# Performance work log

Hardware: AMD Instinct MI355X
Metric: run time of the kernel (lower is better)

The kernel has to match this reference:

```python
import jax, jax.numpy as jnp
import numpy as np


def _isotonic_nonincreasing(y):
    """argmin_{v1>=...>=vn} ||v - y||^2 (PAV solution) via the exact min-max
    formula v[i] = min_{j<=i} max_{k>=i} mean(y[j:k+1]), vectorized O(n^2)."""
    n = y.shape[0]
    S = jnp.concatenate([jnp.zeros(1, y.dtype), jnp.cumsum(y)])  # prefix sums, [n+1]
    j = jnp.arange(n)[:, None]
    k = jnp.arange(n)[None, :]
    den = (k - j + 1).astype(y.dtype)
    # A[j,k] = mean(y[j:k+1]); entries with k<j are never read (see masking argument below)
    A = (S[k + 1] - S[j]) / jnp.where(den > 0, den, jnp.ones((), y.dtype))
    # Mrev[j,i] = max_{k'>=i} A[j,k']; for queries i>=j only valid entries participate
    Mrev = jnp.flip(jax.lax.cummax(jnp.flip(A, 1), axis=1), 1)
    # C[i,i] = min_{j<=i} Mrev[j,i]
    C = jax.lax.cummin(Mrev, axis=0)
    return jnp.diagonal(C)


def _soft_rank_row(z):
    """torchsort.soft_rank (l2 regularization, ascending) on a 1-D vector:
    projection of z onto the permutahedron of (1..n)."""
    n = z.shape[0]
    perm = jnp.argsort(-z)                # descending sort
    s = z[perm]
    w = jnp.arange(n, 0, -1).astype(z.dtype)   # rho = [n, n-1, ..., 1]
    dual = _isotonic_nonincreasing(s - w)
    primal = s - dual
    return jnp.zeros_like(z).at[perm].set(primal)  # undo the sort


def soft_rank(x, regularization_strength=1.0):
    # x: [rows, n]; rank each row over its last dim
    return jax.vmap(_soft_rank_row)(x / regularization_strength)


def setup_inputs() -> dict:
    key = jax.random.key(0)
    ks = jax.random.split(key, 7)
    B, D_IN, H, D_OUT = 4096, 512, 2048, 1

    def lin(kw, kb, fan_in, fan_out):
        lim = 1.0 / np.sqrt(fan_in)  # torch nn.Linear default init
        W = jax.random.uniform(kw, (fan_in, fan_out), jnp.float32, -lim, lim)
        b = jax.random.uniform(kb, (fan_out,), jnp.float32, -lim, lim)
        return W, b

    x = jax.random.normal(ks[0], (B, D_IN), jnp.float32)
    W1, b1 = lin(ks[1], ks[2], D_IN, H)
    W2, b2 = lin(ks[3], ks[4], H, H)
    W3, b3 = lin(ks[5], ks[6], H, D_OUT)
    return {"x": x, "W1": W1, "b1": b1, "W2": W2, "b2": b2, "W3": W3, "b3": b3}


def reference(x, W1, b1, W2, b2, W3, b3):
    # fc stack; Dropout is identity in eval mode
    h = jax.nn.relu(x @ W1 + b1)
    h = jax.nn.relu(h @ W2 + b2)
    scores = h @ W3 + b3                       # [B, D_OUT]
    rank = soft_rank(scores.T, 1.0)            # [D_OUT, B], ranks across the batch
    return rank, scores
```

## Files before the change

### kernel.cpp

```cpp
#include <hip/hip_runtime.h>
#include <hip/hip_bf16.h>

typedef float f32x4 __attribute__((ext_vector_type(4)));
typedef __bf16 bf16x8 __attribute__((ext_vector_type(8)));

#define AS3(p) ((__attribute__((address_space(3))) void*)(p))
#define AS1(p) ((const __attribute__((address_space(1))) void*)(p))

__device__ __forceinline__ unsigned short f2bf(float f) {
    unsigned u = __float_as_uint(f);
    return (unsigned short)((u + 0x7fffu + ((u >> 16) & 1u)) >> 16);
}

__device__ __forceinline__ unsigned long long sort_key(float v, int idx) {
    unsigned ub = __float_as_uint(v);
    unsigned m  = (ub & 0x80000000u) ? ~ub : (ub | 0x80000000u);
    return ((unsigned long long)(~m) << 12) | (unsigned)idx;
}

__global__ __launch_bounds__(256) void prep_all(
    const float* __restrict__ x, unsigned short* __restrict__ xb,
    const float* __restrict__ W1, unsigned short* __restrict__ W1t,
    const float* __restrict__ W2, unsigned short* __restrict__ W2t,
    float* __restrict__ sc, int* __restrict__ posg)
{
    __shared__ float tile[64][65];
    const int bx = blockIdx.x;
    const int t = threadIdx.x;

    if (bx < 1024) {
        int i = bx * 2048 + t * 8;
        float4 v0 = *(const float4*)(x + i);
        float4 v1 = *(const float4*)(x + i + 4);
        ushort4 o0 = { f2bf(v0.x), f2bf(v0.y), f2bf(v0.z), f2bf(v0.w) };
        ushort4 o1 = { f2bf(v1.x), f2bf(v1.y), f2bf(v1.z), f2bf(v1.w) };
        *(ushort4*)(xb + i)     = o0;
        *(ushort4*)(xb + i + 4) = o1;
        return;
    }
    if (bx == 2304) {
        float4 z = {0.f, 0.f, 0.f, 0.f};
        int4 zi = {0, 0, 0, 0};
        #pragma unroll
        for (int i = 0; i < 4; ++i) {
            *(float4*)(sc + t * 16 + i * 4)  = z;
            *(int4*)(posg + t * 16 + i * 4)  = zi;
        }
        return;
    }
    int idx = bx - 1024;
    int ty = idx >> 5;
    int txi = idx & 31;
    const float* W; unsigned short* Wt; int K, N, by;
    if (ty < 8) { W = W1; Wt = W1t; K = 512;  N = 2048; by = ty; }
    else        { W = W2; Wt = W2t; K = 2048; N = 2048; by = ty - 8; }

    const int col4 = t & 15;
    const int row  = t >> 4;
    #pragma unroll
    for (int i = 0; i < 4; ++i) {
        int r = row + i * 16;
        float4 v = *(const float4*)(W + (size_t)(by * 64 + r) * N + txi * 64 + col4 * 4);
        tile[r][col4 * 4 + 0] = v.x;
        tile[r][col4 * 4 + 1] = v.y;
        tile[r][col4 * 4 + 2] = v.z;
        tile[r][col4 * 4 + 3] = v.w;
    }
    __syncthreads();
    #pragma unroll
    for (int i = 0; i < 4; ++i) {
        int r = row + i * 16;
        ushort4 o = { f2bf(tile[col4 * 4 + 0][r]), f2bf(tile[col4 * 4 + 1][r]),
                      f2bf(tile[col4 * 4 + 2][r]), f2bf(tile[col4 * 4 + 3][r]) };
        *(ushort4*)(Wt + (size_t)(txi * 64 + r) * K + by * 64 + col4 * 4) = o;
    }
}

template <int MODE>
__global__ __launch_bounds__(512, 4) void gemm_bf16_mfma(
    const unsigned short* __restrict__ A, const unsigned short* __restrict__ Bt,
    const float* __restrict__ bias, unsigned short* __restrict__ Cbf,
    const float* __restrict__ w3, float* __restrict__ scores,
    int M, int N, int K)
{
    __shared__ unsigned short As[128 * 128];
    __shared__ unsigned short Bs[128 * 128];

    const int tid = threadIdx.x;
    const int wave = tid >> 6, lane = tid & 63;
    const int bn = blockIdx.x, bm = blockIdx.y;
    const int wm = (wave & 1) * 64, wn = (wave >> 1) * 32;

    const unsigned short* Ablk = A  + (size_t)(bm * 128) * K;
    const unsigned short* Bblk = Bt + (size_t)(bn * 128) * K;

    const int rl4 = lane >> 4;
    const int ch  = lane & 15;

    f32x4 acc[4][2] = {};

    for (int k0 = 0; k0 < K; k0 += 128) {
        #pragma unroll
        for (int s2 = 0; s2 < 4; ++s2) {
            int r0 = wave * 16 + s2 * 4;
            int ra = r0 + rl4;
            int gc = (ch ^ (ra & 15)) * 8;
            __builtin_amdgcn_global_load_lds(
                AS1(Ablk + (size_t)ra * K + k0 + gc), AS3(As + r0 * 128), 16, 0, 0);
            __builtin_amdgcn_global_load_lds(
                AS1(Bblk + (size_t)ra * K + k0 + gc), AS3(Bs + r0 * 128), 16, 0, 0);
        }
        __syncthreads();

        #pragma unroll
        for (int s = 0; s < 4; ++s) {
            const int rsw = ((s * 4 + (lane >> 4)) ^ (lane & 15)) * 8;
            bf16x8 a[4], b[2];
            #pragma unroll
            for (int mt = 0; mt < 4; ++mt)
                a[mt] = *(const bf16x8*)(As + (wm + mt * 16 + (lane & 15)) * 128 + rsw);
            #pragma unroll
            for (int nt = 0; nt < 2; ++nt)
                b[nt] = *(const bf16x8*)(Bs + (wn + nt * 16 + (lane & 15)) * 128 + rsw);
            #pragma unroll
            for (int mt = 0; mt < 4; ++mt)
                #pragma unroll
                for (int nt = 0; nt < 2; ++nt)
                    acc[mt][nt] = __builtin_amdgcn_mfma_f32_16x16x32_bf16(
                        a[mt], b[nt], acc[mt][nt], 0, 0, 0);
        }
        __syncthreads();
    }

    const int cm0 = bm * 128 + wm;
    const int cn0 = bn * 128 + wn;
    const int lc = lane & 15;
    const int lr = (lane >> 4) * 4;

    if (MODE == 0) {
        #pragma unroll
        for (int nt = 0; nt < 2; ++nt) {
            float bv = bias[cn0 + nt * 16 + lc];
            #pragma unroll
            for (int mt = 0; mt < 4; ++mt)
                #pragma unroll
                for (int r = 0; r < 4; ++r) {
                    float v = fmaxf(acc[mt][nt][r] + bv, 0.0f);
                    size_t idx = (size_t)(cm0 + mt * 16 + lr + r) * N + cn0 + nt * 16 + lc;
                    Cbf[idx] = f2bf(v);
                }
        }
    } else {
        float bv[2], w3v[2];
        #pragma unroll
        for (int nt = 0; nt < 2; ++nt) {
            bv[nt]  = bias[cn0 + nt * 16 + lc];
            w3v[nt] = w3[cn0 + nt * 16 + lc];
        }
        #pragma unroll
        for (int mt = 0; mt < 4; ++mt)
            #pragma unroll
            for (int r = 0; r < 4; ++r) {
                float p = 0.0f;
                #pragma unroll
                for (int nt = 0; nt < 2; ++nt)
                    p += fmaxf(acc[mt][nt][r] + bv[nt], 0.0f) * w3v[nt];
                p += __shfl_xor(p, 1);
                p += __shfl_xor(p, 2);
                p += __shfl_xor(p, 4);
                p += __shfl_xor(p, 8);
                if (lc == 0)
                    atomicAdd(&scores[cm0 + mt * 16 + lr + r], p);
            }
    }
}

__global__ __launch_bounds__(256) void rank_count(
    const float* __restrict__ sc, const float* __restrict__ b3,
    float* __restrict__ out_scores, int* __restrict__ posg)
{
    __shared__ unsigned long long kj[256];
    const int t = threadIdx.x;
    const int bi = blockIdx.x, bj = blockIdx.y;
    const int i = bi * 256 + t;
    const float b3v = b3[0];

    {
        int j = bj * 256 + t;
        kj[t] = sort_key(sc[j] + b3v, j);
    }
    float vi = sc[i] + b3v;
    if (bj == 0) out_scores[i] = vi;
    const unsigned long long mykey = sort_key(vi, i);
    __syncthreads();

    int cnt = 0;
    #pragma unroll 32
    for (int j = 0; j < 256; ++j)
        cnt += (kj[j] < mykey) ? 1 : 0;
    atomicAdd(&posg[i], cnt);
}

__global__ __launch_bounds__(1024) void pav_fill(
    const float* __restrict__ scores, const float* __restrict__ b3,
    const int* __restrict__ posg, float* __restrict__ rank_out)
{
    constexpr int n = 4096;
    __shared__ __align__(16) unsigned char lds[32768 + 16384 + 8192 + 512];
    double* bsum           = (double*)lds;
    float*  svals          = (float*)(lds + 32768);
    unsigned short* bstart = (unsigned short*)(lds + 49152);
    unsigned short* cnt    = (unsigned short*)(lds + 57344);

    const int tid = threadIdx.x;
    const float b3v = b3[0];

    {
        const int t = tid << 2;
        int4 p4 = *(const int4*)(posg + t);
        float4 s4 = *(const float4*)(scores + t);
        svals[p4.x] = s4.x + b3v;
        svals[p4.y] = s4.y + b3v;
        svals[p4.z] = s4.z + b3v;
        svals[p4.w] = s4.w + b3v;
    }
    __syncthreads();

    if (tid < 256) {
        const int base = tid << 4;
        float vv[16];
        *(float4*)(vv + 0)  = *(const float4*)(svals + base + 0);
        *(float4*)(vv + 4)  = *(const float4*)(svals + base + 4);
        *(float4*)(vv + 8)  = *(const float4*)(svals + base + 8);
        *(float4*)(vv + 12) = *(const float4*)(svals + base + 12);
        int sp = 0;
        double tsum = 0.0; int tstart = 0;
        #pragma unroll
        for (int s = 0; s < 16; ++s) {
            const int i = base + s;
            double csum = (double)vv[s] - (double)(n - i);
            int cs = i;
            const int ce = i + 1;
            while (sp > 0 &&
                   tsum * (double)(ce - cs) <= csum * (double)(cs - tstart)) {
                csum += tsum; cs = tstart; --sp;
                if (sp > 0) { tsum = bsum[base + sp - 1]; tstart = bstart[base + sp - 1]; }
            }
            bsum[base + sp] = csum;
            bstart[base + sp] = (unsigned short)cs;
            tsum = csum; tstart = cs; ++sp;
        }
        cnt[tid] = (unsigned short)sp;
    }
    __syncthreads();

    #pragma unroll 1
    for (int r = 0; r < 8; ++r) {
        const int m = 128 >> r;
        if (tid < m) {
            const int W  = 16 << r;
            const int L  = tid * (W << 1);
            const int Rb = L + W;
            int sp = cnt[L >> 4];
            const int cr = cnt[Rb >> 4];
            double tsum = bsum[L + sp - 1];
            int tstart = bstart[L + sp - 1];
            for (int j = 0; j < cr; ++j) {
                double csum = bsum[Rb + j];
                int cs = (int)bstart[Rb + j];
                const int ce = (j + 1 < cr) ? (int)bstart[Rb + j + 1] : (Rb + W);
                while (sp > 0 &&
                       tsum * (double)(ce - cs) <= csum * (double)(cs - tstart)) {
                    csum += tsum; cs = tstart; --sp;
                    if (sp > 0) { tsum = bsum[L + sp - 1]; tstart = bstart[L + sp - 1]; }
                }
                bsum[L + sp] = csum;
                bstart[L + sp] = (unsigned short)cs;
                tsum = csum; tstart = cs; ++sp;
            }
            cnt[L >> 4] = (unsigned short)sp;
        }
        __syncthreads();
    }

    const int nb = (int)cnt[0];
    {
        const int t = tid << 2;
        int4 p4 = *(const int4*)(posg + t);
        float4 o;
        int pa[4] = { p4.x, p4.y, p4.z, p4.w };
        float oa[4];
        #pragma unroll
        for (int e = 0; e < 4; ++e) {
            const int p = pa[e];
            int lo = 0, hi = nb - 1;
            while (lo < hi) {
                int mid = (lo + hi + 1) >> 1;
                if ((int)bstart[mid] <= p) lo = mid; else hi = mid - 1;
            }
            const int bs = (int)bstart[lo];
            const int be = (lo + 1 < nb) ? (int)bstart[lo + 1] : n;
            oa[e] = svals[p] - (float)(bsum[lo] / (double)(be - bs));
        }
        o.x = oa[0]; o.y = oa[1]; o.z = oa[2]; o.w = oa[3];
        *(float4*)(rank_out + t) = o;
    }
}

extern "C" void kernel_launch(void* const* d_in, const int* in_sizes, int n_in,
                              void* d_out, int out_size, void* d_ws, size_t ws_size,
                              hipStream_t stream) {
    const float* x  = (const float*)d_in[0];
    const float* W1 = (const float*)d_in[1];
    const float* b1 = (const float*)d_in[2];
    const float* W2 = (const float*)d_in[3];
    const float* b2 = (const float*)d_in[4];
    const float* W3 = (const float*)d_in[5];
    const float* b3 = (const float*)d_in[6];
    float* out = (float*)d_out;

    const int B = 4096, D_IN = 512, H = 2048;

    char* ws = (char*)d_ws;
    unsigned short* h1  = (unsigned short*)(ws);
    unsigned short* xb  = (unsigned short*)(ws + (16u << 20));
    unsigned short* W1t = (unsigned short*)(ws + (20u << 20));
    unsigned short* W2t = (unsigned short*)(ws + (22u << 20));
    float*          sc  = (float*)(ws + (30u << 20));
    int*            posg= (int*)(ws + (30u << 20) + 16384);

    prep_all<<<2305, 256, 0, stream>>>(x, xb, W1, W1t, W2, W2t, sc, posg);

    gemm_bf16_mfma<0><<<dim3(H / 128, B / 128), 512, 0, stream>>>(
        xb, W1t, b1, h1, nullptr, nullptr, B, H, D_IN);
    gemm_bf16_mfma<1><<<dim3(H / 128, B / 128), 512, 0, stream>>>(
        h1, W2t, b2, nullptr, W3, sc, B, H, H);

    rank_count<<<dim3(B / 256, B / 256), 256, 0, stream>>>(sc, b3, out + B, posg);
    pav_fill<<<1, 1024, 0, stream>>>(sc, b3, posg, out);
}
```

Baseline: 150.6 us.

## Double-buffer GEMM LDS tiles with BK=64 and XCD-aware block remapping

Restructures the bf16 MFMA GEMM main loop from a single 128-wide K tile to two ping-pong 64-wide K buffers. The next tile's global-to-LDS loads are issued before computing the current one, with explicit vmcnt waits and barriers. It also remaps block IDs so consecutive blocks spread across the XCDs, and raises wave priority during MFMA sections. The aim is to hide global load latency behind compute and improve L2 locality, at the cost of more barriers per K step and fragile hand-counted waitcnt values.

```diff
diff --git a/kernel.cpp b/kernel.cpp
--- a/kernel.cpp
+++ b/kernel.cpp
@@ -76,6 +76,12 @@
     }
 }
 
+#define GB_WAITV(n) { asm volatile("s_waitcnt vmcnt(" #n ")" ::: "memory"); \
+                      __builtin_amdgcn_sched_barrier(0); }
+#define GB_BAR()    { __builtin_amdgcn_sched_barrier(0);                    \
+                      __builtin_amdgcn_s_barrier();                         \
+                      __builtin_amdgcn_sched_barrier(0); }
+
 template <int MODE>
 __global__ __launch_bounds__(512, 4) void gemm_bf16_mfma(
     const unsigned short* __restrict__ A, const unsigned short* __restrict__ Bt,
@@ -83,79 +89,117 @@
     const float* __restrict__ w3, float* __restrict__ scores,
     int M, int N, int K)
 {
-    __shared__ unsigned short As[128 * 128];
-    __shared__ unsigned short Bs[128 * 128];
+    __shared__ __align__(16) unsigned short As[2][128 * 64];
+    __shared__ __align__(16) unsigned short Bs[2][128 * 64];
 
     const int tid = threadIdx.x;
     const int wave = tid >> 6, lane = tid & 63;
-    const int bn = blockIdx.x, bm = blockIdx.y;
+
+    const unsigned nwg = gridDim.x * gridDim.y;
+    const unsigned bid = blockIdx.y * gridDim.x + blockIdx.x;
+    const unsigned sbid = (bid & 7u) * (nwg >> 3) + (bid >> 3);
+    const int bn = sbid % gridDim.x;
+    const int bm = sbid / gridDim.x;
+
     const int wm = (wave & 1) * 64, wn = (wave >> 1) * 32;
 
     const unsigned short* Ablk = A  + (size_t)(bm * 128) * K;
     const unsigned short* Bblk = Bt + (size_t)(bn * 128) * K;
 
     const int rl4 = lane >> 4;
-    const int ch  = lane & 15;
+    const int lc  = lane & 15;
+
+    const int srow = lane >> 3;
+    const int sgc  = ((lane & 7) ^ srow) << 3;
 
     f32x4 acc[4][2] = {};
 
-    for (int k0 = 0; k0 < K; k0 += 128) {
-        #pragma unroll
-        for (int s2 = 0; s2 < 4; ++s2) {
-            int r0 = wave * 16 + s2 * 4;
-            int ra = r0 + rl4;
-            int gc = (ch ^ (ra & 15)) * 8;
-            __builtin_amdgcn_global_load_lds(
-                AS1(Ablk + (size_t)ra * K + k0 + gc), AS3(As + r0 * 128), 16, 0, 0);
-            __builtin_amdgcn_global_load_lds(
-                AS1(Bblk + (size_t)ra * K + k0 + gc), AS3(Bs + r0 * 128), 16, 0, 0);
-        }
-        __syncthreads();
-
-        #pragma unroll
-        for (int s = 0; s < 4; ++s) {
-            const int rsw = ((s * 4 + (lane >> 4)) ^ (lane & 15)) * 8;
-            bf16x8 a[4], b[2];
-            #pragma unroll
-            for (int mt = 0; mt < 4; ++mt)
-                a[mt] = *(const bf16x8*)(As + (wm + mt * 16 + (lane & 15)) * 128 + rsw);
-            #pragma unroll
-            for (int nt = 0; nt < 2; ++nt)
-                b[nt] = *(const bf16x8*)(Bs + (wn + nt * 16 + (lane & 15)) * 128 + rsw);
-            #pragma unroll
-            for (int mt = 0; mt < 4; ++mt)
-                #pragma unroll
-                for (int nt = 0; nt < 2; ++nt)
-                    acc[mt][nt] = __builtin_amdgcn_mfma_f32_16x16x32_bf16(
-                        a[mt], b[nt], acc[mt][nt], 0, 0, 0);
-        }
-        __syncthreads();
-    }
+    const int nt = K >> 6;
+
+    #define GB_STAGE(k0, Ad, Bd)                                               \
+        _Pragma("unroll")                                                      \
+        for (int l = 0; l < 2; ++l) {                                          \
+            const int ra = l * 64 + wave * 8 + srow;                           \
+            const int lo = (l * 64 + wave * 8) * 64;                           \
+            __builtin_amdgcn_global_load_lds(                                  \
+                AS1(Ablk + (size_t)ra * K + (k0) + sgc), AS3((Ad) + lo), 16, 0, 0); \
+            __builtin_amdgcn_global_load_lds(                                  \
+                AS1(Bblk + (size_t)ra * K + (k0) + sgc), AS3((Bd) + lo), 16, 0, 0); \
+        }
+
+    #define GB_COMPUTE(Ab, Bb)                                                 \
+        __builtin_amdgcn_s_setprio(1);                                         \
+        _Pragma("unroll")                                                      \
+        for (int s = 0; s < 2; ++s) {                                          \
+            const int rsw = (((s * 4 + rl4) ^ (lc & 7)) << 3);                 \
+            bf16x8 a[4], b[2];                                                 \
+            _Pragma("unroll")                                                  \
+            for (int mt = 0; mt < 4; ++mt)                                     \
+                a[mt] = *(const bf16x8*)((Ab) + (wm + mt * 16 + lc) * 64 + rsw);\
+            _Pragma("unroll")                                                  \
+            for (int nt2 = 0; nt2 < 2; ++nt2)                                  \
+                b[nt2] = *(const bf16x8*)((Bb) + (wn + nt2 * 16 + lc) * 64 + rsw);\
+            _Pragma("unroll")                                                  \
+            for (int mt = 0; mt < 4; ++mt)                                     \
+                _Pragma("unroll")                                              \
+                for (int nt2 = 0; nt2 < 2; ++nt2)                              \
+                    acc[mt][nt2] = __builtin_amdgcn_mfma_f32_16x16x32_bf16(    \
+                        a[mt], b[nt2], acc[mt][nt2], 0, 0, 0);                 \
+        }                                                                      \
+        __builtin_amdgcn_s_setprio(0);
+
+    GB_STAGE(0, As[0], Bs[0]);
+
+    for (int t = 0; t < nt; t += 2) {
+        if (t + 1 < nt) {
+            GB_STAGE((t + 1) << 6, As[1], Bs[1]);
+            GB_WAITV(4);
+        } else {
+            GB_WAITV(0);
+        }
+        GB_BAR();
+        GB_COMPUTE(As[0], Bs[0]);
+        GB_BAR();
+
+        if (t + 1 < nt) {
+            if (t + 2 < nt) {
+                GB_STAGE((t + 2) << 6, As[0], Bs[0]);
+                GB_WAITV(4);
+            } else {
+                GB_WAITV(0);
+            }
+            GB_BAR();
+            GB_COMPUTE(As[1], Bs[1]);
+            GB_BAR();
+        }
+    }
+
+    #undef GB_STAGE
+    #undef GB_COMPUTE
 
     const int cm0 = bm * 128 + wm;
     const int cn0 = bn * 128 + wn;
-    const int lc = lane & 15;
     const int lr = (lane >> 4) * 4;
 
     if (MODE == 0) {
         #pragma unroll
-        for (int nt = 0; nt < 2; ++nt) {
-            float bv = bias[cn0 + nt * 16 + lc];
+        for (int nt2 = 0; nt2 < 2; ++nt2) {
+            float bv = bias[cn0 + nt2 * 16 + lc];
             #pragma unroll
             for (int mt = 0; mt < 4; ++mt)
                 #pragma unroll
                 for (int r = 0; r < 4; ++r) {
-                    float v = fmaxf(acc[mt][nt][r] + bv, 0.0f);
-                    size_t idx = (size_t)(cm0 + mt * 16 + lr + r) * N + cn0 + nt * 16 + lc;
+                    float v = fmaxf(acc[mt][nt2][r] + bv, 0.0f);
+                    size_t idx = (size_t)(cm0 + mt * 16 + lr + r) * N + cn0 + nt2 * 16 + lc;
                     Cbf[idx] = f2bf(v);
                 }
         }
     } else {
         float bv[2], w3v[2];
         #pragma unroll
-        for (int nt = 0; nt < 2; ++nt) {
-            bv[nt]  = bias[cn0 + nt * 16 + lc];
-            w3v[nt] = w3[cn0 + nt * 16 + lc];
+        for (int nt2 = 0; nt2 < 2; ++nt2) {
+            bv[nt2]  = bias[cn0 + nt2 * 16 + lc];
+            w3v[nt2] = w3[cn0 + nt2 * 16 + lc];
         }
         #pragma unroll
         for (int mt = 0; mt < 4; ++mt)
@@ -163,8 +207,8 @@
             for (int r = 0; r < 4; ++r) {
                 float p = 0.0f;
                 #pragma unroll
-                for (int nt = 0; nt < 2; ++nt)
-                    p += fmaxf(acc[mt][nt][r] + bv[nt], 0.0f) * w3v[nt];
+                for (int nt2 = 0; nt2 < 2; ++nt2)
+                    p += fmaxf(acc[mt][nt2][r] + bv[nt2], 0.0f) * w3v[nt2];
                 p += __shfl_xor(p, 1);
                 p += __shfl_xor(p, 2);
                 p += __shfl_xor(p, 4);
```

Result: no change. 149.7 us (-0.6%).

## Triple-buffer GEMM K-loop with async LDS prefetch and larger 256x128 tiles

Applied to the files above, without the earlier changes.

Rewrites the bf16 MFMA GEMM to use 256x128 output tiles with a 64-wide K step. LDS is triple-buffered, and the loads for tile t+2 are split into two halves that are interleaved with the MFMA blocks, synchronised by vmcnt waits and a single barrier per step. Block IDs are remapped so that groups of 8 workgroups map to contiguous tile regions, and s_setprio is raised around the MFMA phases. The aim is to hide global-load latency and raise arithmetic intensity per block, at the cost of more registers and LDS, which lowers occupancy to 2 blocks per CU.

```diff
diff --git a/kernel.cpp b/kernel.cpp
--- a/kernel.cpp
+++ b/kernel.cpp
@@ -76,86 +76,155 @@
     }
 }
 
+#define GB_WAITV(n) { asm volatile("s_waitcnt vmcnt(" #n ")" ::: "memory"); \
+                      __builtin_amdgcn_sched_barrier(0); }
+
 template <int MODE>
-__global__ __launch_bounds__(512, 4) void gemm_bf16_mfma(
+__global__ __launch_bounds__(512, 2) void gemm_bf16_mfma(
     const unsigned short* __restrict__ A, const unsigned short* __restrict__ Bt,
     const float* __restrict__ bias, unsigned short* __restrict__ Cbf,
     const float* __restrict__ w3, float* __restrict__ scores,
     int M, int N, int K)
 {
-    __shared__ unsigned short As[128 * 128];
-    __shared__ unsigned short Bs[128 * 128];
+    __shared__ __align__(16) unsigned short lds3[3][384 * 64];
+    constexpr int BOFF = 256 * 64;
 
     const int tid = threadIdx.x;
     const int wave = tid >> 6, lane = tid & 63;
-    const int bn = blockIdx.x, bm = blockIdx.y;
-    const int wm = (wave & 1) * 64, wn = (wave >> 1) * 32;
-
-    const unsigned short* Ablk = A  + (size_t)(bm * 128) * K;
+
+    const unsigned nwg = gridDim.x * gridDim.y;
+    const unsigned bid = blockIdx.y * gridDim.x + blockIdx.x;
+    const unsigned sbid = (bid & 7u) * (nwg >> 3) + (bid >> 3);
+    const int bn = sbid % gridDim.x;
+    const int bm = sbid / gridDim.x;
+
+    const int wm = (wave >> 1) * 64;
+    const int wn = (wave & 1) * 64;
+
+    const unsigned short* Ablk = A  + (size_t)(bm * 256) * K;
     const unsigned short* Bblk = Bt + (size_t)(bn * 128) * K;
 
+    const int lc  = lane & 15;
     const int rl4 = lane >> 4;
-    const int ch  = lane & 15;
-
-    f32x4 acc[4][2] = {};
-
-    for (int k0 = 0; k0 < K; k0 += 128) {
-        #pragma unroll
-        for (int s2 = 0; s2 < 4; ++s2) {
-            int r0 = wave * 16 + s2 * 4;
-            int ra = r0 + rl4;
-            int gc = (ch ^ (ra & 15)) * 8;
-            __builtin_amdgcn_global_load_lds(
-                AS1(Ablk + (size_t)ra * K + k0 + gc), AS3(As + r0 * 128), 16, 0, 0);
-            __builtin_amdgcn_global_load_lds(
-                AS1(Bblk + (size_t)ra * K + k0 + gc), AS3(Bs + r0 * 128), 16, 0, 0);
-        }
-        __syncthreads();
-
-        #pragma unroll
-        for (int s = 0; s < 4; ++s) {
-            const int rsw = ((s * 4 + (lane >> 4)) ^ (lane & 15)) * 8;
-            bf16x8 a[4], b[2];
-            #pragma unroll
-            for (int mt = 0; mt < 4; ++mt)
-                a[mt] = *(const bf16x8*)(As + (wm + mt * 16 + (lane & 15)) * 128 + rsw);
-            #pragma unroll
-            for (int nt = 0; nt < 2; ++nt)
-                b[nt] = *(const bf16x8*)(Bs + (wn + nt * 16 + (lane & 15)) * 128 + rsw);
-            #pragma unroll
-            for (int mt = 0; mt < 4; ++mt)
+    const int srow = lane >> 3;
+    const int sgc  = ((lane & 7) ^ srow) << 3;
+
+    f32x4 acc[4][4] = {};
+    const int nt = K >> 6;
+
+    unsigned short *Ac = lds3[0], *An = lds3[1], *Asp = lds3[2];
+
+    #define STG_P1(k0, D) {                                                    \
+        _Pragma("unroll")                                                      \
+        for (int i = 0; i < 2; ++i) {                                          \
+            const int ra = wave * 32 + i * 8 + srow;                           \
+            __builtin_amdgcn_global_load_lds(                                  \
+                AS1(Ablk + (size_t)ra * K + (k0) + sgc),                       \
+                AS3((D) + (wave * 32 + i * 8) * 64), 16, 0, 0);                \
+        }                                                                      \
+        {                                                                      \
+            const int rb = wave * 16 + srow;                                   \
+            __builtin_amdgcn_global_load_lds(                                  \
+                AS1(Bblk + (size_t)rb * K + (k0) + sgc),                       \
+                AS3((D) + BOFF + (wave * 16) * 64), 16, 0, 0);                 \
+        } }
+    #define STG_P2(k0, D) {                                                    \
+        _Pragma("unroll")                                                      \
+        for (int i = 2; i < 4; ++i) {                                          \
+            const int ra = wave * 32 + i * 8 + srow;                           \
+            __builtin_amdgcn_global_load_lds(                                  \
+                AS1(Ablk + (size_t)ra * K + (k0) + sgc),                       \
+                AS3((D) + (wave * 32 + i * 8) * 64), 16, 0, 0);                \
+        }                                                                      \
+        {                                                                      \
+            const int rb = wave * 16 + 8 + srow;                               \
+            __builtin_amdgcn_global_load_lds(                                  \
+                AS1(Bblk + (size_t)rb * K + (k0) + sgc),                       \
+                AS3((D) + BOFF + (wave * 16 + 8) * 64), 16, 0, 0);             \
+        } }
+
+    STG_P1(0, Ac);  STG_P2(0, Ac);
+    STG_P1(64, An); STG_P2(64, An);
+
+    for (int t = 0; t < nt; ++t) {
+        if (t < nt - 1) { GB_WAITV(6); } else { GB_WAITV(0); }
+        __builtin_amdgcn_s_barrier();
+
+        const bool pf = (t + 2 < nt);
+        const int kpf = (t + 2) << 6;
+
+        if (pf) STG_P1(kpf, Asp);
+        bf16x8 a[4][2], b[2][2];
+        #pragma unroll
+        for (int mt = 0; mt < 4; ++mt)
+            #pragma unroll
+            for (int kk = 0; kk < 2; ++kk)
+                a[mt][kk] = *(const bf16x8*)(
+                    Ac + (wm + mt * 16 + lc) * 64 + (((kk * 4 + rl4) ^ (lc & 7)) << 3));
+        #pragma unroll
+        for (int n2 = 0; n2 < 2; ++n2)
+            #pragma unroll
+            for (int kk = 0; kk < 2; ++kk)
+                b[n2][kk] = *(const bf16x8*)(
+                    Ac + BOFF + (wn + n2 * 16 + lc) * 64 + (((kk * 4 + rl4) ^ (lc & 7)) << 3));
+        __builtin_amdgcn_s_setprio(1);
+        #pragma unroll
+        for (int mt = 0; mt < 4; ++mt)
+            #pragma unroll
+            for (int n2 = 0; n2 < 2; ++n2)
                 #pragma unroll
-                for (int nt = 0; nt < 2; ++nt)
-                    acc[mt][nt] = __builtin_amdgcn_mfma_f32_16x16x32_bf16(
-                        a[mt], b[nt], acc[mt][nt], 0, 0, 0);
-        }
-        __syncthreads();
-    }
-
-    const int cm0 = bm * 128 + wm;
+                for (int kk = 0; kk < 2; ++kk)
+                    acc[mt][n2] = __builtin_amdgcn_mfma_f32_16x16x32_bf16(
+                        a[mt][kk], b[n2][kk], acc[mt][n2], 0, 0, 0);
+        __builtin_amdgcn_s_setprio(0);
+
+        if (pf) STG_P2(kpf, Asp);
+        #pragma unroll
+        for (int n2 = 0; n2 < 2; ++n2)
+            #pragma unroll
+            for (int kk = 0; kk < 2; ++kk)
+                b[n2][kk] = *(const bf16x8*)(
+                    Ac + BOFF + (wn + 32 + n2 * 16 + lc) * 64 + (((kk * 4 + rl4) ^ (lc & 7)) << 3));
+        __builtin_amdgcn_s_setprio(1);
+        #pragma unroll
+        for (int mt = 0; mt < 4; ++mt)
+            #pragma unroll
+            for (int n2 = 0; n2 < 2; ++n2)
+                #pragma unroll
+                for (int kk = 0; kk < 2; ++kk)
+                    acc[mt][2 + n2] = __builtin_amdgcn_mfma_f32_16x16x32_bf16(
+                        a[mt][kk], b[n2][kk], acc[mt][2 + n2], 0, 0, 0);
+        __builtin_amdgcn_s_setprio(0);
+
+        unsigned short* tmp = Ac; Ac = An; An = Asp; Asp = tmp;
+    }
+
+    #undef STG_P1
+    #undef STG_P2
+
+    const int cm0 = bm * 256 + wm;
     const int cn0 = bn * 128 + wn;
-    const int lc = lane & 15;
     const int lr = (lane >> 4) * 4;
 
     if (MODE == 0) {
         #pragma unroll
-        for (int nt = 0; nt < 2; ++nt) {
-            float bv = bias[cn0 + nt * 16 + lc];
+        for (int j = 0; j < 4; ++j) {
+            float bv = bias[cn0 + j * 16 + lc];
             #pragma unroll
             for (int mt = 0; mt < 4; ++mt)
                 #pragma unroll
                 for (int r = 0; r < 4; ++r) {
-                    float v = fmaxf(acc[mt][nt][r] + bv, 0.0f);
-                    size_t idx = (size_t)(cm0 + mt * 16 + lr + r) * N + cn0 + nt * 16 + lc;
+                    float v = fmaxf(acc[mt][j][r] + bv, 0.0f);
+                    size_t idx = (size_t)(cm0 + mt * 16 + lr + r) * N + cn0 + j * 16 + lc;
                     Cbf[idx] = f2bf(v);
                 }
         }
     } else {
-        float bv[2], w3v[2];
-        #pragma unroll
-        for (int nt = 0; nt < 2; ++nt) {
-            bv[nt]  = bias[cn0 + nt * 16 + lc];
-            w3v[nt] = w3[cn0 + nt * 16 + lc];
+        float bv[4], w3v[4];
+        #pragma unroll
+        for (int j = 0; j < 4; ++j) {
+            bv[j]  = bias[cn0 + j * 16 + lc];
+            w3v[j] = w3[cn0 + j * 16 + lc];
         }
         #pragma unroll
         for (int mt = 0; mt < 4; ++mt)
@@ -163,8 +232,8 @@
             for (int r = 0; r < 4; ++r) {
                 float p = 0.0f;
                 #pragma unroll
-                for (int nt = 0; nt < 2; ++nt)
-                    p += fmaxf(acc[mt][nt][r] + bv[nt], 0.0f) * w3v[nt];
+                for (int j = 0; j < 4; ++j)
+                    p += fmaxf(acc[mt][j][r] + bv[j], 0.0f) * w3v[j];
                 p += __shfl_xor(p, 1);
                 p += __shfl_xor(p, 2);
                 p += __shfl_xor(p, 4);
@@ -331,9 +400,9 @@
 
     prep_all<<<2305, 256, 0, stream>>>(x, xb, W1, W1t, W2, W2t, sc, posg);
 
-    gemm_bf16_mfma<0><<<dim3(H / 128, B / 128), 512, 0, stream>>>(
+    gemm_bf16_mfma<0><<<dim3(H / 128, B / 256), 512, 0, stream>>>(
         xb, W1t, b1, h1, nullptr, nullptr, B, H, D_IN);
-    gemm_bf16_mfma<1><<<dim3(H / 128, B / 128), 512, 0, stream>>>(
+    gemm_bf16_mfma<1><<<dim3(H / 128, B / 256), 512, 0, stream>>>(
         h1, W2t, b2, nullptr, W3, sc, B, H, H);
 
     rank_count<<<dim3(B / 256, B / 256), 256, 0, stream>>>(sc, b3, out + B, posg);
```

After: 140.2 us, median of 2. -6.9%, faster.
